# Kernel tuning notes

Measured on AMD Instinct MI355X. Metric: run time of the kernel, lower is better.

## Reference

```python
import jax, jax.numpy as jnp
import numpy as np

# frontier sizes per layer (input -> output) and edges per block
N = [400000, 120000, 20000, 4000]
E = [1800000, 200000, 20000]
IN_FEATS, N_HIDDEN, N_CLASSES = 128, 256, 47


def setup_inputs() -> dict:
    key = jax.random.key(0)
    ks = jax.random.split(key, 16)
    inp = {}
    inp["x"] = jax.random.normal(ks[0], (N[0], IN_FEATS), dtype=jnp.float32)
    # block edge lists: src in [0, N[l]), dst in [0, N[l+1))
    for l in range(3):
        inp[f"src{l}"] = jax.random.randint(ks[1 + 2 * l], (E[l],), 0, N[l], dtype=jnp.int32)
        inp[f"dst{l}"] = jax.random.randint(ks[2 + 2 * l], (E[l],), 0, N[l + 1], dtype=jnp.int32)
    dims = [(IN_FEATS, N_HIDDEN), (N_HIDDEN, N_HIDDEN), (N_HIDDEN, N_CLASSES)]
    for l, (din, dout) in enumerate(dims):
        scale = 1.0 / np.sqrt(din)
        inp[f"Ws{l}"] = jax.random.normal(ks[7 + 3 * l], (din, dout), dtype=jnp.float32) * scale
        inp[f"Wn{l}"] = jax.random.normal(ks[8 + 3 * l], (din, dout), dtype=jnp.float32) * scale
        inp[f"b{l}"] = jnp.zeros((dout,), dtype=jnp.float32)
    return inp


def sage_layer(h, src, dst, n_dst, Ws, Wn, b):
    # mean aggregation over incoming edges (gather -> segment-reduce)
    msgs = h[src]  # [E, din]
    neigh_sum = jax.ops.segment_sum(msgs, dst, num_segments=n_dst)
    deg = jax.ops.segment_sum(jnp.ones((dst.shape[0], 1), h.dtype), dst, num_segments=n_dst)
    neigh_mean = neigh_sum / jnp.maximum(deg, 1.0)
    # DGL block convention: dst nodes are the first n_dst src nodes
    return h[:n_dst] @ Ws + neigh_mean @ Wn + b


def reference(x, src0, dst0, src1, dst1, src2, dst2,
              Ws0, Wn0, b0, Ws1, Wn1, b1, Ws2, Wn2, b2):
    h = jax.nn.relu(sage_layer(x, src0, dst0, N[1], Ws0, Wn0, b0))
    h = jax.nn.relu(sage_layer(h, src1, dst1, N[2], Ws1, Wn1, b1))
    h = sage_layer(h, src2, dst2, N[3], Ws2, Wn2, b2)
    return h
```

## Files before the change

kernel.cpp:

```cpp
#include <hip/hip_runtime.h>
#include <hip/hip_bf16.h>

typedef __hip_bfloat16 bf16;
typedef __attribute__((ext_vector_type(8))) short short8;
typedef __attribute__((ext_vector_type(4))) float float4v;

#define N1 120000
#define N2 20000
#define N3 4000
#define E0 1800000
#define E1 200000
#define E2 20000
#define D_IN 128
#define D_HID 256
#define D_OUT 47

__device__ __forceinline__ void stv(float* p, float v) { *p = v; }
__device__ __forceinline__ void stv(bf16* p, float v) { *p = __float2bfloat16(v); }

__device__ __forceinline__ unsigned short f2bu(float v) {
    union { bf16 h; unsigned short u; } c;
    c.h = __float2bfloat16(v);
    return c.u;
}
__device__ __forceinline__ short f2bs(float v) { return (short)f2bu(v); }
__device__ __forceinline__ float bu2f(unsigned short u) { return __uint_as_float(((unsigned)u) << 16); }

__device__ __forceinline__ short8 load8(const bf16* p) {
    union { uint4 u; short8 s; } r;
    r.u = *(const uint4*)p;
    return r.s;
}
__device__ __forceinline__ short8 load8(const float* p) {
    float4 a = *(const float4*)p;
    float4 b = *(const float4*)(p + 4);
    short8 s;
    s[0] = f2bs(a.x); s[1] = f2bs(a.y); s[2] = f2bs(a.z); s[3] = f2bs(a.w);
    s[4] = f2bs(b.x); s[5] = f2bs(b.y); s[6] = f2bs(b.z); s[7] = f2bs(b.w);
    return s;
}

__global__ __launch_bounds__(256) void convert_x(const float* __restrict__ x,
                                                 bf16* __restrict__ xb, int n8) {
    int i = blockIdx.x * blockDim.x + threadIdx.x;
    if (i >= n8) return;
    const float* p = x + (size_t)i * 8;
    float4 a = *(const float4*)p;
    float4 b = *(const float4*)(p + 4);
    union { uint4 u; short s[8]; } o;
    o.s[0] = f2bs(a.x); o.s[1] = f2bs(a.y); o.s[2] = f2bs(a.z); o.s[3] = f2bs(a.w);
    o.s[4] = f2bs(b.x); o.s[5] = f2bs(b.y); o.s[6] = f2bs(b.z); o.s[7] = f2bs(b.w);
    *(uint4*)(xb + (size_t)i * 8) = o.u;
}

__global__ void wt_batch(const float* W0s, const float* W0n, const float* W1s,
                         const float* W1n, const float* W2s, const float* W2n,
                         bf16* T0s, bf16* T0n, bf16* T1s, bf16* T1n, bf16* T2s, bf16* T2n) {
    int i = blockIdx.x * blockDim.x + threadIdx.x;
    const float* W; bf16* T; int K, N, j;
    if      (i <  32768) { W = W0s; T = T0s; K = 128; N = 256; j = i; }
    else if (i <  65536) { W = W0n; T = T0n; K = 128; N = 256; j = i - 32768; }
    else if (i < 131072) { W = W1s; T = T1s; K = 256; N = 256; j = i - 65536; }
    else if (i < 196608) { W = W1n; T = T1n; K = 256; N = 256; j = i - 131072; }
    else if (i < 208896) { W = W2s; T = T2s; K = 256; N = 47;  j = i - 196608; }
    else if (i < 221184) { W = W2n; T = T2n; K = 256; N = 47;  j = i - 208896; }
    else return;
    int n = j / K, k = j - n * K;
    float v = (n < N) ? W[(size_t)k * N + n] : 0.f;
    T[j] = __float2bfloat16(v);
}

__global__ void hist_batch(const int* __restrict__ d0, const int* __restrict__ d1,
                           const int* __restrict__ d2, int* __restrict__ c0,
                           int* __restrict__ c1, int* __restrict__ c2) {
    int i = blockIdx.x * blockDim.x + threadIdx.x;
    if (i < E0) atomicAdd(&c0[d0[i]], 1);
    else if (i < E0 + E1) atomicAdd(&c1[d1[i - E0]], 1);
    else if (i < E0 + E1 + E2) atomicAdd(&c2[d2[i - E0 - E1]], 1);
}

__global__ __launch_bounds__(256) void scan_chunk_batch(
    const int* __restrict__ c0, const int* __restrict__ c1, const int* __restrict__ c2,
    int* __restrict__ r0, int* __restrict__ r1, int* __restrict__ r2, int* __restrict__ bsum) {
    __shared__ int sd[256];
    int b = blockIdx.x, t = threadIdx.x;
    const int* cnt; int* out; int* bs; int n, cb;
    if (b < 118)      { cnt = c0; out = r0; bs = bsum;       n = N1; cb = b; }
    else if (b < 138) { cnt = c1; out = r1; bs = bsum + 128; n = N2; cb = b - 118; }
    else              { cnt = c2; out = r2; bs = bsum + 256; n = N3; cb = b - 138; }
    int base = cb * 1024 + t * 4;
    int v[4]; int s = 0;
    #pragma unroll
    for (int j = 0; j < 4; j++) { int i = base + j; v[j] = (i < n) ? cnt[i] : 0; s += v[j]; }
    sd[t] = s;
    __syncthreads();
    for (int off = 1; off < 256; off <<= 1) {
        int x = (t >= off) ? sd[t - off] : 0;
        __syncthreads();
        sd[t] += x;
        __syncthreads();
    }
    int run = sd[t] - s;
    #pragma unroll
    for (int j = 0; j < 4; j++) { int i = base + j; if (i < n) out[i] = run; run += v[j]; }
    if (t == 255) bs[cb] = sd[255];
}

__global__ __launch_bounds__(256) void scan_bsum_batch(int* __restrict__ bsum,
        int* __restrict__ r0, int* __restrict__ r1, int* __restrict__ r2) {
    __shared__ int sd[256];
    int l = blockIdx.x, t = threadIdx.x;
    int B = (l == 0) ? 118 : (l == 1 ? 20 : 4);
    int* bs = bsum + l * 128;
    int s = (t < B) ? bs[t] : 0;
    sd[t] = s;
    __syncthreads();
    for (int off = 1; off < 256; off <<= 1) {
        int x = (t >= off) ? sd[t - off] : 0;
        __syncthreads();
        sd[t] += x;
        __syncthreads();
    }
    if (t < B) bs[t] = sd[t] - s;
    if (t == 255) {
        if (l == 0) r0[N1] = sd[255];
        else if (l == 1) r1[N2] = sd[255];
        else r2[N3] = sd[255];
    }
}

__global__ void scan_add_batch(int* __restrict__ r0, int* __restrict__ r1,
                               int* __restrict__ r2, const int* __restrict__ bsum) {
    int i = blockIdx.x * blockDim.x + threadIdx.x;
    if (i < N1) r0[i] += bsum[i >> 10];
    else if (i < N1 + N2) { int j = i - N1; r1[j] += bsum[128 + (j >> 10)]; }
    else if (i < N1 + N2 + N3) { int j = i - N1 - N2; r2[j] += bsum[256 + (j >> 10)]; }
}

__global__ void csr_fill_batch(const int* __restrict__ s0, const int* __restrict__ d0,
                               const int* __restrict__ s1, const int* __restrict__ d1,
                               const int* __restrict__ s2, const int* __restrict__ d2,
                               int* __restrict__ c0, int* __restrict__ c1, int* __restrict__ c2,
                               const int* __restrict__ r0, const int* __restrict__ r1,
                               const int* __restrict__ r2, int* __restrict__ col0,
                               int* __restrict__ col1, int* __restrict__ col2) {
    int i = blockIdx.x * blockDim.x + threadIdx.x;
    if (i < E0) {
        int d = d0[i];
        col0[r0[d] + atomicSub(&c0[d], 1) - 1] = s0[i];
    } else if (i < E0 + E1) {
        int e = i - E0; int d = d1[e];
        col1[r1[d] + atomicSub(&c1[d], 1) - 1] = s1[e];
    } else if (i < E0 + E1 + E2) {
        int e = i - E0 - E1; int d = d2[e];
        col2[r2[d] + atomicSub(&c2[d], 1) - 1] = s2[e];
    }
}

template <int DIN, typename T>
__global__ __launch_bounds__(256) void gather_mean(const T* __restrict__ h,
        const int* __restrict__ rp, const int* __restrict__ col,
        int n_dst, bf16* __restrict__ agg) {
    int gw = (blockIdx.x * blockDim.x + threadIdx.x) >> 6;
    int lane = threadIdx.x & 63;
    if (gw >= n_dst) return;
    int beg = rp[gw], end = rp[gw + 1];
    constexpr int VP = DIN / 64;
    float s[VP] = {};

    auto accum = [&](int srcn) {
        const T* hp = h + (size_t)srcn * DIN + lane * VP;
        if constexpr (sizeof(T) == 4) {
            float2 v = *(const float2*)hp;
            s[0] += v.x; s[1] += v.y;
        } else if constexpr (VP == 2) {
            union { unsigned u; unsigned short us[2]; } r;
            r.u = *(const unsigned*)hp;
            s[0] += bu2f(r.us[0]); s[1] += bu2f(r.us[1]);
        } else {
            union { uint2 u; unsigned short us[4]; } r;
            r.u = *(const uint2*)hp;
            #pragma unroll
            for (int j = 0; j < 4; j++) s[j] += bu2f(r.us[j]);
        }
    };

    int e = beg;
    for (; e + 3 < end; e += 4) {
        int a0 = col[e], a1 = col[e + 1], a2 = col[e + 2], a3 = col[e + 3];
        accum(a0); accum(a1); accum(a2); accum(a3);
    }
    for (; e < end; ++e) accum(col[e]);

    float inv = 1.f / fmaxf((float)(end - beg), 1.f);
    #pragma unroll
    for (int j = 0; j < VP; j++) s[j] *= inv;

    bf16* ap = agg + (size_t)gw * DIN + lane * VP;
    if constexpr (VP == 2) {
        ushort2 o; o.x = f2bu(s[0]); o.y = f2bu(s[1]);
        *(ushort2*)ap = o;
    } else {
        ushort4 o; o.x = f2bu(s[0]); o.y = f2bu(s[1]); o.z = f2bu(s[2]); o.w = f2bu(s[3]);
        *(ushort4*)ap = o;
    }
}

template <typename TA, typename TC, bool RELU>
__global__ __launch_bounds__(256) void gemm_mfma(
    const TA* __restrict__ A, const bf16* __restrict__ Mn,
    const bf16* __restrict__ Wst, const bf16* __restrict__ Wnt,
    const float* __restrict__ bias, TC* __restrict__ C,
    int M, int Nstore, int Npad, int K) {
    __shared__ short As[128][48];
    __shared__ short Bs[128][48];

    int tid = threadIdx.x;
    int m0 = blockIdx.x * 128;
    int n0 = blockIdx.y * 128;
    int lane = tid & 63, wid = tid >> 6;
    int wm = (wid & 1) * 64, wn = (wid >> 1) * 64;
    int l15 = lane & 15, quad = lane >> 4;

    float4v acc[4][4] = {};

    int nsteps = (2 * K) >> 5;
    int r = tid >> 2, c = (tid & 3) << 3;
    for (int s = 0; s < nsteps; ++s) {
        int ks = s << 5;
        bool self = ks < K;
        int ko = self ? ks : ks - K;
        #pragma unroll
        for (int it = 0; it < 2; ++it) {
            int rr = r + it * 64;
            {
                int gm = m0 + rr;
                short8 v = (short8)0;
                if (gm < M) {
                    if (self) v = load8(A  + (size_t)gm * K + ko + c);
                    else      v = load8(Mn + (size_t)gm * K + ko + c);
                }
                *(short8*)&As[rr][c] = v;
            }
            {
                int gn = n0 + rr;
                short8 w = (short8)0;
                if (gn < Npad) {
                    const bf16* Wp = self ? Wst : Wnt;
                    w = load8(Wp + (size_t)gn * K + ko + c);
                }
                *(short8*)&Bs[rr][c] = w;
            }
        }
        __syncthreads();
        short8 af[4], bfr[4];
        #pragma unroll
        for (int i = 0; i < 4; ++i)
            af[i] = *(const short8*)&As[wm + i * 16 + l15][quad * 8];
        #pragma unroll
        for (int j = 0; j < 4; ++j)
            bfr[j] = *(const short8*)&Bs[wn + j * 16 + l15][quad * 8];
        #pragma unroll
        for (int i = 0; i < 4; ++i)
            #pragma unroll
            for (int j = 0; j < 4; ++j)
                acc[i][j] = __builtin_amdgcn_mfma_f32_16x16x32_bf16(af[i], bfr[j], acc[i][j], 0, 0, 0);
        __syncthreads();
    }

    #pragma unroll
    for (int i = 0; i < 4; ++i) {
        #pragma unroll
        for (int j = 0; j < 4; ++j) {
            int gn = n0 + wn + j * 16 + l15;
            if (gn >= Nstore) continue;
            float bv = bias[gn];
            #pragma unroll
            for (int rr = 0; rr < 4; ++rr) {
                int gm = m0 + wm + i * 16 + quad * 4 + rr;
                if (gm >= M) continue;
                float v = acc[i][j][rr] + bv;
                if (RELU) v = fmaxf(v, 0.f);
                stv(&C[(size_t)gm * Nstore + gn], v);
            }
        }
    }
}

extern "C" void kernel_launch(void* const* d_in, const int* in_sizes, int n_in,
                              void* d_out, int out_size, void* d_ws, size_t ws_size,
                              hipStream_t stream) {
    const float* x    = (const float*)d_in[0];
    const int*  src0 = (const int*)d_in[1];
    const int*  dst0 = (const int*)d_in[2];
    const int*  src1 = (const int*)d_in[3];
    const int*  dst1 = (const int*)d_in[4];
    const int*  src2 = (const int*)d_in[5];
    const int*  dst2 = (const int*)d_in[6];
    const float* Ws0 = (const float*)d_in[7];
    const float* Wn0 = (const float*)d_in[8];
    const float* b0  = (const float*)d_in[9];
    const float* Ws1 = (const float*)d_in[10];
    const float* Wn1 = (const float*)d_in[11];
    const float* b1  = (const float*)d_in[12];
    const float* Ws2 = (const float*)d_in[13];
    const float* Wn2 = (const float*)d_in[14];
    const float* b2  = (const float*)d_in[15];
    float* out = (float*)d_out;

    char* W = (char*)d_ws;
    int* cnt0  = (int*)(W + 0);
    int* cnt1  = (int*)(W + 480000);
    int* cnt2  = (int*)(W + 560000);
    int* rp0   = (int*)(W + 576000);
    int* rp1   = (int*)(W + 1056004);
    int* rp2   = (int*)(W + 1136008);
    int* col0  = (int*)(W + 1152016);
    int* col1  = (int*)(W + 8352016);
    int* col2  = (int*)(W + 9152016);
    int* bsum  = (int*)(W + 9232016);
    bf16* Wst0 = (bf16*)(W + 9233552);
    bf16* Wnt0 = (bf16*)(W + 9299088);
    bf16* Wst1 = (bf16*)(W + 9364624);
    bf16* Wnt1 = (bf16*)(W + 9495696);
    bf16* Wst2 = (bf16*)(W + 9626768);
    bf16* Wnt2 = (bf16*)(W + 9651344);

    const size_t BASE = 9676032;
    const bool use_xb = ws_size >= (size_t)205000000;
    bf16* xb = (bf16*)(W + BASE);
    size_t agg0_off = BASE + (use_xb ? 102400000 : 0);
    bf16* agg0 = (bf16*)(W + agg0_off);
    bf16* h1   = (bf16*)(W + agg0_off + 30720000);
    bf16* agg1 = (bf16*)(W + BASE);
    bf16* h2   = (bf16*)(W + BASE + 10240000);
    bf16* agg2 = (bf16*)(W + BASE + 20480000);

    hipMemsetAsync(W, 0, 576000, stream);
    if (use_xb) {
        int n8 = 400000 * D_IN / 8;
        convert_x<<<(n8 + 255) / 256, 256, 0, stream>>>(x, xb, n8);
    }
    wt_batch<<<(221184 + 255) / 256, 256, 0, stream>>>(Ws0, Wn0, Ws1, Wn1, Ws2, Wn2,
                                                       Wst0, Wnt0, Wst1, Wnt1, Wst2, Wnt2);
    const int ETOT = E0 + E1 + E2;
    hist_batch<<<(ETOT + 255) / 256, 256, 0, stream>>>(dst0, dst1, dst2, cnt0, cnt1, cnt2);
    scan_chunk_batch<<<142, 256, 0, stream>>>(cnt0, cnt1, cnt2, rp0, rp1, rp2, bsum);
    scan_bsum_batch<<<3, 256, 0, stream>>>(bsum, rp0, rp1, rp2);
    scan_add_batch<<<(N1 + N2 + N3 + 255) / 256, 256, 0, stream>>>(rp0, rp1, rp2, bsum);
    csr_fill_batch<<<(ETOT + 255) / 256, 256, 0, stream>>>(src0, dst0, src1, dst1, src2, dst2,
                                                           cnt0, cnt1, cnt2, rp0, rp1, rp2,
                                                           col0, col1, col2);

    if (use_xb) {
        gather_mean<D_IN, bf16><<<(N1 + 3) / 4, 256, 0, stream>>>(xb, rp0, col0, N1, agg0);
        dim3 grid((N1 + 127) / 128, 2);
        gemm_mfma<bf16, bf16, true><<<grid, 256, 0, stream>>>(xb, agg0, Wst0, Wnt0, b0, h1, N1, 256, 256, 128);
    } else {
        gather_mean<D_IN, float><<<(N1 + 3) / 4, 256, 0, stream>>>(x, rp0, col0, N1, agg0);
        dim3 grid((N1 + 127) / 128, 2);
        gemm_mfma<float, bf16, true><<<grid, 256, 0, stream>>>(x, agg0, Wst0, Wnt0, b0, h1, N1, 256, 256, 128);
    }

    gather_mean<D_HID, bf16><<<(N2 + 3) / 4, 256, 0, stream>>>(h1, rp1, col1, N2, agg1);
    {
        dim3 grid((N2 + 127) / 128, 2);
        gemm_mfma<bf16, bf16, true><<<grid, 256, 0, stream>>>(h1, agg1, Wst1, Wnt1, b1, h2, N2, 256, 256, 256);
    }

    gather_mean<D_HID, bf16><<<(N3 + 3) / 4, 256, 0, stream>>>(h2, rp2, col2, N3, agg2);
    {
        dim3 grid((N3 + 127) / 128, 1);
        gemm_mfma<bf16, float, false><<<grid, 256, 0, stream>>>(h2, agg2, Wst2, Wnt2, b2, out, N3, 47, 48, 256);
    }
}
```

Baseline: 754.3 us.

## Build CSR via two-level bucketed binning instead of global atomics

Replaces the global per-node atomic histogram, three-kernel scan and atomic scatter fill with a bucketed CSR build. Destinations are grouped into 512-node buckets: a shared-memory bucket histogram, a small scan, a binning pass that packs src and local dst into buffered shared-memory chunks, then one block per bucket builds the local CSR. The aim is to cut scattered global atomics and random writes. It adds an intermediate edge buffer and needs src to fit in 23 bits after the pack, and bin_pass runs only 62 blocks, which may limit parallelism.

```diff
diff --git a/kernel.cpp b/kernel.cpp
--- a/kernel.cpp
+++ b/kernel.cpp
@@ -14,6 +14,11 @@
 #define D_IN 128
 #define D_HID 256
 #define D_OUT 47
+
+#define NB0 235
+#define NB1 40
+#define NB2 8
+#define BCAP 32
 
 __device__ __forceinline__ void stv(float* p, float v) { *p = v; }
 __device__ __forceinline__ void stv(bf16* p, float v) { *p = __float2bfloat16(v); }
@@ -70,29 +75,33 @@
     T[j] = __float2bfloat16(v);
 }
 
-__global__ void hist_batch(const int* __restrict__ d0, const int* __restrict__ d1,
-                           const int* __restrict__ d2, int* __restrict__ c0,
-                           int* __restrict__ c1, int* __restrict__ c2) {
-    int i = blockIdx.x * blockDim.x + threadIdx.x;
-    if (i < E0) atomicAdd(&c0[d0[i]], 1);
-    else if (i < E0 + E1) atomicAdd(&c1[d1[i - E0]], 1);
-    else if (i < E0 + E1 + E2) atomicAdd(&c2[d2[i - E0 - E1]], 1);
-}
-
-__global__ __launch_bounds__(256) void scan_chunk_batch(
-    const int* __restrict__ c0, const int* __restrict__ c1, const int* __restrict__ c2,
-    int* __restrict__ r0, int* __restrict__ r1, int* __restrict__ r2, int* __restrict__ bsum) {
+__global__ __launch_bounds__(256) void bucket_hist(
+    const int* __restrict__ d0, const int* __restrict__ d1, const int* __restrict__ d2,
+    int* __restrict__ bc) {
+    __shared__ int h[NB0];
+    int b = blockIdx.x, t = threadIdx.x;
+    const int* dst; int* bcl; int e0, e1, nb;
+    if (b < 440)      { dst = d0; bcl = bc;       nb = NB0; e0 = b * 4096;         e1 = min(e0 + 4096, E0); }
+    else if (b < 489) { dst = d1; bcl = bc + 256; nb = NB1; e0 = (b - 440) * 4096; e1 = min(e0 + 4096, E1); }
+    else              { dst = d2; bcl = bc + 512; nb = NB2; e0 = (b - 489) * 4096; e1 = min(e0 + 4096, E2); }
+    for (int i = t; i < nb; i += 256) h[i] = 0;
+    __syncthreads();
+    for (int e = e0 + t; e < e1; e += 256) atomicAdd(&h[dst[e] >> 9], 1);
+    __syncthreads();
+    for (int i = t; i < nb; i += 256) { int v = h[i]; if (v) atomicAdd(&bcl[i], v); }
+}
+
+__global__ __launch_bounds__(256) void bucket_scan(
+    const int* __restrict__ bc, int* __restrict__ bb, int* __restrict__ bu,
+    int* __restrict__ rp0, int* __restrict__ rp1, int* __restrict__ rp2) {
     __shared__ int sd[256];
-    int b = blockIdx.x, t = threadIdx.x;
-    const int* cnt; int* out; int* bs; int n, cb;
-    if (b < 118)      { cnt = c0; out = r0; bs = bsum;       n = N1; cb = b; }
-    else if (b < 138) { cnt = c1; out = r1; bs = bsum + 128; n = N2; cb = b - 118; }
-    else              { cnt = c2; out = r2; bs = bsum + 256; n = N3; cb = b - 138; }
-    int base = cb * 1024 + t * 4;
-    int v[4]; int s = 0;
-    #pragma unroll
-    for (int j = 0; j < 4; j++) { int i = base + j; v[j] = (i < n) ? cnt[i] : 0; s += v[j]; }
-    sd[t] = s;
+    int l = blockIdx.x, t = threadIdx.x;
+    int nb = (l == 0) ? NB0 : (l == 1 ? NB1 : NB2);
+    const int* bcl = bc + l * 256;
+    int* bbl = bb + l * 256;
+    int* bul = bu + l * 256;
+    int v = (t < nb) ? bcl[t] : 0;
+    sd[t] = v;
     __syncthreads();
     for (int off = 1; off < 256; off <<= 1) {
         int x = (t >= off) ? sd[t - off] : 0;
@@ -100,60 +109,104 @@
         sd[t] += x;
         __syncthreads();
     }
-    int run = sd[t] - s;
-    #pragma unroll
-    for (int j = 0; j < 4; j++) { int i = base + j; if (i < n) out[i] = run; run += v[j]; }
-    if (t == 255) bs[cb] = sd[255];
-}
-
-__global__ __launch_bounds__(256) void scan_bsum_batch(int* __restrict__ bsum,
-        int* __restrict__ r0, int* __restrict__ r1, int* __restrict__ r2) {
-    __shared__ int sd[256];
-    int l = blockIdx.x, t = threadIdx.x;
-    int B = (l == 0) ? 118 : (l == 1 ? 20 : 4);
-    int* bs = bsum + l * 128;
-    int s = (t < B) ? bs[t] : 0;
-    sd[t] = s;
+    int ex = sd[t] - v;
+    if (t < nb) { bbl[t] = ex; bul[t] = ex; }
+    if (t == 0) {
+        if (l == 0) rp0[N1] = E0;
+        else if (l == 1) rp1[N2] = E1;
+        else rp2[N3] = E2;
+    }
+}
+
+__global__ __launch_bounds__(256) void bin_pass(
+    const int* __restrict__ s0, const int* __restrict__ d0,
+    const int* __restrict__ s1, const int* __restrict__ d1,
+    const int* __restrict__ s2, const int* __restrict__ d2,
+    int* __restrict__ bu, int* __restrict__ eb0, int* __restrict__ eb1,
+    int* __restrict__ eb2) {
+    __shared__ int cnt[NB0];
+    __shared__ int data[NB0 * BCAP];
+    int b = blockIdx.x, t = threadIdx.x;
+    const int *src, *dst; int *cur, *eb; int nb, e0, e1;
+    if (b < 48)      { src = s0; dst = d0; cur = bu;       eb = eb0; nb = NB0; e0 = b * 37888;        e1 = min(e0 + 37888, E0); }
+    else if (b < 60) { src = s1; dst = d1; cur = bu + 256; eb = eb1; nb = NB1; e0 = (b - 48) * 17408; e1 = min(e0 + 17408, E1); }
+    else             { src = s2; dst = d2; cur = bu + 512; eb = eb2; nb = NB2; e0 = (b - 60) * 10240; e1 = min(e0 + 10240, E2); }
+    for (int i = t; i < nb; i += 256) cnt[i] = 0;
+    __syncthreads();
+    for (int rb = e0; rb < e1; rb += 1024) {
+        #pragma unroll
+        for (int j = 0; j < 4; j++) {
+            int e = rb + j * 256 + t;
+            if (e < e1) {
+                int d = dst[e];
+                int gb = d >> 9;
+                int pk = (src[e] << 9) | (d & 511);
+                int pos = atomicAdd(&cnt[gb], 1);
+                if (pos < BCAP) data[gb * BCAP + pos] = pk;
+                else { int p = atomicAdd(&cur[gb], 1); eb[p] = pk; }
+            }
+        }
+        __syncthreads();
+        if (t < nb) {
+            int c = cnt[t];
+            if (c >= BCAP) {
+                int p = atomicAdd(&cur[t], BCAP);
+                #pragma unroll
+                for (int j = 0; j < BCAP; j++) eb[p + j] = data[t * BCAP + j];
+                cnt[t] = 0;
+            }
+        }
+        __syncthreads();
+    }
+    if (t < nb) {
+        int c = min(cnt[t], BCAP);
+        if (c > 0) {
+            int p = atomicAdd(&cur[t], c);
+            for (int j = 0; j < c; j++) eb[p + j] = data[t * BCAP + j];
+        }
+    }
+}
+
+__global__ __launch_bounds__(256) void local_csr(
+    const int* __restrict__ bb, const int* __restrict__ bc,
+    const int* __restrict__ eb0, const int* __restrict__ eb1, const int* __restrict__ eb2,
+    int* __restrict__ rp0, int* __restrict__ rp1, int* __restrict__ rp2,
+    int* __restrict__ col0, int* __restrict__ col1, int* __restrict__ col2) {
+    __shared__ int lcnt[512];
+    __shared__ int lrp[512];
+    __shared__ int sscan[256];
+    int b = blockIdx.x, t = threadIdx.x;
+    const int *eb; int *rp, *col; int bkt, Nl, loff;
+    if (b < 235)      { bkt = b;       eb = eb0; rp = rp0; col = col0; Nl = N1; loff = 0; }
+    else if (b < 275) { bkt = b - 235; eb = eb1; rp = rp1; col = col1; Nl = N2; loff = 256; }
+    else              { bkt = b - 275; eb = eb2; rp = rp2; col = col2; Nl = N3; loff = 512; }
+    int base = bb[loff + bkt];
+    int cb   = bc[loff + bkt];
+    int dbase = bkt << 9;
+    int nloc = min(512, Nl - dbase);
+    lcnt[t] = 0; lcnt[t + 256] = 0;
+    __syncthreads();
+    for (int i = t; i < cb; i += 256) atomicAdd(&lcnt[eb[base + i] & 511], 1);
+    __syncthreads();
+    int a0 = lcnt[2 * t], a1 = lcnt[2 * t + 1];
+    sscan[t] = a0 + a1;
     __syncthreads();
     for (int off = 1; off < 256; off <<= 1) {
-        int x = (t >= off) ? sd[t - off] : 0;
-        __syncthreads();
-        sd[t] += x;
-        __syncthreads();
-    }
-    if (t < B) bs[t] = sd[t] - s;
-    if (t == 255) {
-        if (l == 0) r0[N1] = sd[255];
-        else if (l == 1) r1[N2] = sd[255];
-        else r2[N3] = sd[255];
-    }
-}
-
-__global__ void scan_add_batch(int* __restrict__ r0, int* __restrict__ r1,
-                               int* __restrict__ r2, const int* __restrict__ bsum) {
-    int i = blockIdx.x * blockDim.x + threadIdx.x;
-    if (i < N1) r0[i] += bsum[i >> 10];
-    else if (i < N1 + N2) { int j = i - N1; r1[j] += bsum[128 + (j >> 10)]; }
-    else if (i < N1 + N2 + N3) { int j = i - N1 - N2; r2[j] += bsum[256 + (j >> 10)]; }
-}
-
-__global__ void csr_fill_batch(const int* __restrict__ s0, const int* __restrict__ d0,
-                               const int* __restrict__ s1, const int* __restrict__ d1,
-                               const int* __restrict__ s2, const int* __restrict__ d2,
-                               int* __restrict__ c0, int* __restrict__ c1, int* __restrict__ c2,
-                               const int* __restrict__ r0, const int* __restrict__ r1,
-                               const int* __restrict__ r2, int* __restrict__ col0,
-                               int* __restrict__ col1, int* __restrict__ col2) {
-    int i = blockIdx.x * blockDim.x + threadIdx.x;
-    if (i < E0) {
-        int d = d0[i];
-        col0[r0[d] + atomicSub(&c0[d], 1) - 1] = s0[i];
-    } else if (i < E0 + E1) {
-        int e = i - E0; int d = d1[e];
-        col1[r1[d] + atomicSub(&c1[d], 1) - 1] = s1[e];
-    } else if (i < E0 + E1 + E2) {
-        int e = i - E0 - E1; int d = d2[e];
-        col2[r2[d] + atomicSub(&c2[d], 1) - 1] = s2[e];
+        int x = (t >= off) ? sscan[t - off] : 0;
+        __syncthreads();
+        sscan[t] += x;
+        __syncthreads();
+    }
+    int ex = sscan[t] - (a0 + a1);
+    lrp[2 * t] = ex;
+    lrp[2 * t + 1] = ex + a0;
+    __syncthreads();
+    for (int i = t; i < nloc; i += 256) rp[dbase + i] = base + lrp[i];
+    for (int i = t; i < cb; i += 256) {
+        int pk = eb[base + i];
+        int ld = pk & 511;
+        int ofs = atomicSub(&lcnt[ld], 1) - 1;
+        col[base + lrp[ld] + ofs] = pk >> 9;
     }
 }
 
@@ -309,25 +362,27 @@
     float* out = (float*)d_out;
 
     char* W = (char*)d_ws;
-    int* cnt0  = (int*)(W + 0);
-    int* cnt1  = (int*)(W + 480000);
-    int* cnt2  = (int*)(W + 560000);
-    int* rp0   = (int*)(W + 576000);
-    int* rp1   = (int*)(W + 1056004);
-    int* rp2   = (int*)(W + 1136008);
-    int* col0  = (int*)(W + 1152016);
-    int* col1  = (int*)(W + 8352016);
-    int* col2  = (int*)(W + 9152016);
-    int* bsum  = (int*)(W + 9232016);
-    bf16* Wst0 = (bf16*)(W + 9233552);
-    bf16* Wnt0 = (bf16*)(W + 9299088);
-    bf16* Wst1 = (bf16*)(W + 9364624);
-    bf16* Wnt1 = (bf16*)(W + 9495696);
-    bf16* Wst2 = (bf16*)(W + 9626768);
-    bf16* Wnt2 = (bf16*)(W + 9651344);
-
-    const size_t BASE = 9676032;
-    const bool use_xb = ws_size >= (size_t)205000000;
+    int* rp0   = (int*)(W + 0);
+    int* rp1   = (int*)(W + 480004);
+    int* rp2   = (int*)(W + 560008);
+    int* col0  = (int*)(W + 576016);
+    int* col1  = (int*)(W + 7776016);
+    int* col2  = (int*)(W + 8576016);
+    int* eb0   = (int*)(W + 8656016);
+    int* eb1   = (int*)(W + 15856016);
+    int* eb2   = (int*)(W + 16656016);
+    int* bcnt  = (int*)(W + 16736016);
+    int* bbase = (int*)(W + 16739088);
+    int* bcur  = (int*)(W + 16742160);
+    bf16* Wst0 = (bf16*)(W + 16745232);
+    bf16* Wnt0 = (bf16*)(W + 16810768);
+    bf16* Wst1 = (bf16*)(W + 16876304);
+    bf16* Wnt1 = (bf16*)(W + 17007376);
+    bf16* Wst2 = (bf16*)(W + 17138448);
+    bf16* Wnt2 = (bf16*)(W + 17163024);
+
+    const size_t BASE = 17187840;
+    const bool use_xb = ws_size >= (size_t)(BASE + 102400000 + 30720000 + 61440000 + 1024);
     bf16* xb = (bf16*)(W + BASE);
     size_t agg0_off = BASE + (use_xb ? 102400000 : 0);
     bf16* agg0 = (bf16*)(W + agg0_off);
@@ -336,21 +391,19 @@
     bf16* h2   = (bf16*)(W + BASE + 10240000);
     bf16* agg2 = (bf16*)(W + BASE + 20480000);
 
-    hipMemsetAsync(W, 0, 576000, stream);
+    hipMemsetAsync(bcnt, 0, 3072, stream);
     if (use_xb) {
         int n8 = 400000 * D_IN / 8;
         convert_x<<<(n8 + 255) / 256, 256, 0, stream>>>(x, xb, n8);
     }
     wt_batch<<<(221184 + 255) / 256, 256, 0, stream>>>(Ws0, Wn0, Ws1, Wn1, Ws2, Wn2,
                                                        Wst0, Wnt0, Wst1, Wnt1, Wst2, Wnt2);
-    const int ETOT = E0 + E1 + E2;
-    hist_batch<<<(ETOT + 255) / 256, 256, 0, stream>>>(dst0, dst1, dst2, cnt0, cnt1, cnt2);
-    scan_chunk_batch<<<142, 256, 0, stream>>>(cnt0, cnt1, cnt2, rp0, rp1, rp2, bsum);
-    scan_bsum_batch<<<3, 256, 0, stream>>>(bsum, rp0, rp1, rp2);
-    scan_add_batch<<<(N1 + N2 + N3 + 255) / 256, 256, 0, stream>>>(rp0, rp1, rp2, bsum);
-    csr_fill_batch<<<(ETOT + 255) / 256, 256, 0, stream>>>(src0, dst0, src1, dst1, src2, dst2,
-                                                           cnt0, cnt1, cnt2, rp0, rp1, rp2,
-                                                           col0, col1, col2);
+    bucket_hist<<<494, 256, 0, stream>>>(dst0, dst1, dst2, bcnt);
+    bucket_scan<<<3, 256, 0, stream>>>(bcnt, bbase, bcur, rp0, rp1, rp2);
+    bin_pass<<<62, 256, 0, stream>>>(src0, dst0, src1, dst1, src2, dst2,
+                                     bcur, eb0, eb1, eb2);
+    local_csr<<<283, 256, 0, stream>>>(bbase, bcnt, eb0, eb1, eb2,
+                                       rp0, rp1, rp2, col0, col1, col2);
 
     if (use_xb) {
         gather_mean<D_IN, bf16><<<(N1 + 3) / 4, 256, 0, stream>>>(xb, rp0, col0, N1, agg0);
```

After: 812.6 us. 1.08x slower.
